# Optimization experiments

Hardware: AMD Instinct MI355X
Metric: run time of the kernel (lower is better)

Reference implementation:

```python
import jax, jax.numpy as jnp
import numpy as np

EPS = 1e-6
NUM_HEADS = 16

def _rmsnorm(h, w):
    hf = h.astype(jnp.float32)
    var = jnp.mean(hf * hf, axis=-1, keepdims=True)
    return (w * (hf * jax.lax.rsqrt(var + EPS))).astype(h.dtype)

def _rotary(t, cos, sin):
    # t: [B,N,H,hd]; cos/sin: [N, hd//2]
    tf = t.astype(jnp.float32)
    tr = tf[..., 0::2]
    ti = tf[..., 1::2]
    c = cos[None, :, None, :]
    s = sin[None, :, None, :]
    out_r = tr * c - ti * s
    out_i = tr * s + ti * c
    out = jnp.stack([out_r, out_i], axis=-1).reshape(t.shape)
    return out.astype(t.dtype)

def setup_inputs() -> dict:
    key = jax.random.key(0)
    ks = jax.random.split(key, 8)
    B, N, C = 2, 2048, 1024
    hd = C // NUM_HEADS
    x = jax.random.normal(ks[0], (B, N, C), jnp.float32)
    qkv_w = jax.random.normal(ks[1], (3 * C, C), jnp.float32) * (C ** -0.5)
    q_norm_w = jnp.ones((hd,), jnp.float32)
    k_norm_w = jnp.ones((hd,), jnp.float32)
    proj_w = jax.random.normal(ks[2], (C, C), jnp.float32) * (C ** -0.5)
    proj_b = jnp.zeros((C,), jnp.float32)
    # rotary freqs_cis = exp(i * theta): unit-magnitude cos/sin
    inv_freq = 1.0 / (10000.0 ** (jnp.arange(0, hd, 2, dtype=jnp.float32) / hd))
    ang = jnp.arange(N, dtype=jnp.float32)[:, None] * inv_freq[None, :]
    pos_cos = jnp.cos(ang)
    pos_sin = jnp.sin(ang)
    mask = jnp.tril(jnp.ones((N, N), dtype=bool))
    return {"x": x, "qkv_w": qkv_w, "q_norm_w": q_norm_w, "k_norm_w": k_norm_w,
            "proj_w": proj_w, "proj_b": proj_b, "pos_cos": pos_cos,
            "pos_sin": pos_sin, "mask": mask}

def reference(x, qkv_w, q_norm_w, k_norm_w, proj_w, proj_b, pos_cos, pos_sin, mask):
    B, N, C = x.shape
    H = NUM_HEADS
    hd = C // H
    qkv = (x @ qkv_w.T).reshape(B, N, 3, H, hd)
    q, k, v = qkv[:, :, 0], qkv[:, :, 1], qkv[:, :, 2]  # [B,N,H,hd]
    q = _rmsnorm(q, q_norm_w)
    k = _rmsnorm(k, k_norm_w)
    q = _rotary(q, pos_cos, pos_sin)
    k = _rotary(k, pos_cos, pos_sin)
    q = q.transpose(0, 2, 1, 3)  # [B,H,N,hd]
    k = k.transpose(0, 2, 1, 3)
    v = v.transpose(0, 2, 1, 3)
    scale = hd ** -0.5
    scores = jnp.einsum('bhqd,bhkd->bhqk', q, k) * scale
    scores = jnp.where(mask[None, None, :, :], scores, jnp.float32(-1e30))
    attn = jax.nn.softmax(scores, axis=-1)
    out = jnp.einsum('bhqk,bhkd->bhqd', attn, v)
    out = out.transpose(0, 2, 1, 3).reshape(B, N, C)
    return out @ proj_w.T + proj_b
```

## Files before the change

### kernel.cpp

```cpp
#include <hip/hip_runtime.h>

using u16 = unsigned short;
using short4v = __attribute__((ext_vector_type(4))) short;
using short8 = __attribute__((ext_vector_type(8))) short;
using floatx4 = __attribute__((ext_vector_type(4))) float;

__device__ __forceinline__ float bf2f(u16 h) {
  union { unsigned int u; float f; } v;
  v.u = ((unsigned int)h) << 16;
  return v.f;
}
__device__ __forceinline__ u16 f2bf(float f) {
  union { float f; unsigned int u; } v;
  v.f = f;
  unsigned int u = v.u;
  return (u16)((u + 0x7FFFu + ((u >> 16) & 1u)) >> 16);
}
__device__ __forceinline__ u16 f2bf_rtz(float f) {
  union { float f; unsigned int u; } v;
  v.f = f;
  return (u16)(v.u >> 16);
}

typedef const __attribute__((address_space(1))) unsigned int* gas_t;
typedef __attribute__((address_space(3))) unsigned int* las_t;
__device__ __forceinline__ void gl_lds16(const u16* g, u16* l) {
  __builtin_amdgcn_global_load_lds((gas_t)(const void*)g, (las_t)(void*)l, 16,
                                   0, 0);
}

#define QSCALE 0.180336880111f
#define EXPBIAS 23.0831206542f

__global__ __launch_bounds__(256) void cvt_all(
    const float* __restrict__ x, const float* __restrict__ wq,
    const float* __restrict__ wp, u16* __restrict__ xb, u16* __restrict__ wqb,
    u16* __restrict__ wpb) {
  int i = blockIdx.x * 256 + threadIdx.x;
  const float* src;
  u16* dst;
  int off;
  if (i < 1048576) {
    src = x; dst = xb; off = i;
  } else if (i < 1048576 + 786432) {
    src = wq; dst = wqb; off = i - 1048576;
  } else {
    src = wp; dst = wpb; off = i - 1835008;
  }
  float4 v = ((const float4*)src)[off];
  ushort4 o;
  o.x = f2bf(v.x);
  o.y = f2bf(v.y);
  o.z = f2bf(v.z);
  o.w = f2bf(v.w);
  ((ushort4*)dst)[off] = o;
}

template <int BIAS, int OUTBF16, int MT>
__global__ __launch_bounds__(256) void gemm_nt(
    const u16* __restrict__ A, const u16* __restrict__ B,
    const float* __restrict__ bias, void* __restrict__ Cout,
    int M, int N, int K) {
  constexpr int ROWS_A = MT * 32;
  __shared__ u16 As[ROWS_A * 32];
  __shared__ u16 Bs[128 * 32];
  const int tid = threadIdx.x;
  const int lane = tid & 63;
  const int wave = tid >> 6;
  const int col = lane & 15;
  const int quad = lane >> 4;
  const int bm = blockIdx.y * ROWS_A;
  const int bn = blockIdx.x * 128;
  const int wm = (wave >> 1) * (MT * 16);
  const int wn = (wave & 1) * 64;

  floatx4 acc[MT][4] = {};

  for (int kb = 0; kb < K; kb += 32) {
    __syncthreads();
#pragma unroll
    for (int c = tid; c < ROWS_A * 4; c += 256)
      gl_lds16(A + (size_t)(bm + (c >> 2)) * K + kb + (c & 3) * 8, As + c * 8);
#pragma unroll
    for (int c = tid; c < 512; c += 256)
      gl_lds16(B + (size_t)(bn + (c >> 2)) * K + kb + (c & 3) * 8, Bs + c * 8);
    __syncthreads();

    short8 af[MT], bfr[4];
#pragma unroll
    for (int i = 0; i < MT; i++)
      af[i] = *(const short8*)(As + (wm + i * 16 + col) * 32 + quad * 8);
#pragma unroll
    for (int i = 0; i < 4; i++)
      bfr[i] = *(const short8*)(Bs + (wn + i * 16 + col) * 32 + quad * 8);
#pragma unroll
    for (int mi = 0; mi < MT; mi++)
#pragma unroll
      for (int ni = 0; ni < 4; ni++)
        acc[mi][ni] = __builtin_amdgcn_mfma_f32_16x16x32_bf16(
            af[mi], bfr[ni], acc[mi][ni], 0, 0, 0);
  }

#pragma unroll
  for (int mi = 0; mi < MT; mi++) {
#pragma unroll
    for (int ni = 0; ni < 4; ni++) {
#pragma unroll
      for (int r = 0; r < 4; r++) {
        int row = bm + wm + mi * 16 + quad * 4 + r;
        int c = bn + wn + ni * 16 + col;
        float v = acc[mi][ni][r];
        if (BIAS) v += bias[c];
        if (OUTBF16)
          ((u16*)Cout)[(size_t)row * N + c] = f2bf(v);
        else
          ((float*)Cout)[(size_t)row * N + c] = v;
      }
    }
  }
}

__global__ __launch_bounds__(256) void rope_v(
    const u16* __restrict__ qkv, const float* __restrict__ qw,
    const float* __restrict__ kw, const float* __restrict__ pcos,
    const float* __restrict__ psin, u16* __restrict__ Qb,
    u16* __restrict__ Kb, u16* __restrict__ Vt) {
  __shared__ u16 T[64 * 68];
  const int bh = blockIdx.x;
  const int n0 = blockIdx.y * 64;
  const int b = bh >> 4, h = bh & 15;
  const int tid = threadIdx.x;
  const int lane = tid & 63;
  const int wave = tid >> 6;

  const float qwl = qw[lane];
  const float kwl = kw[lane];
  for (int tt = 0; tt < 16; tt++) {
    const int n = n0 + wave * 16 + tt;
    const int t = b * 2048 + n;
    const u16* base = qkv + (size_t)t * 3072 + h * 64 + lane;
    float qv = bf2f(base[0]);
    float kv = bf2f(base[1024]);

    float sq = qv * qv, sk = kv * kv;
#pragma unroll
    for (int off = 32; off; off >>= 1) {
      sq += __shfl_xor(sq, off);
      sk += __shfl_xor(sk, off);
    }
    float qn = qv * rsqrtf(sq * (1.0f / 64.0f) + 1e-6f) * qwl;
    float kn = kv * rsqrtf(sk * (1.0f / 64.0f) + 1e-6f) * kwl;

    const int i = lane >> 1;
    const float c = pcos[n * 32 + i];
    const float s = psin[n * 32 + i];
    float qp = __shfl_xor(qn, 1);
    float kp = __shfl_xor(kn, 1);
    float qr, kr;
    if (lane & 1) {
      qr = qp * s + qn * c;
      kr = kp * s + kn * c;
    } else {
      qr = qn * c - qp * s;
      kr = kn * c - kp * s;
    }
    qr *= QSCALE;

    const size_t o = ((size_t)bh * 2048 + n) * 64 + lane;
    Qb[o] = f2bf(qr);
    Kb[o] = f2bf(kr);
  }

  const int q = tid & 7;
  const int r = tid >> 3;
#pragma unroll
  for (int rr = r; rr < 64; rr += 32) {
    short8 v = *(const short8*)(qkv + (size_t)(b * 2048 + n0 + rr) * 3072 +
                                2048 + h * 64 + q * 8);
    *(short8*)&T[rr * 68 + q * 8] = v;
  }
  __syncthreads();
#pragma unroll
  for (int dd = r; dd < 64; dd += 32) {
    short8 o;
#pragma unroll
    for (int j = 0; j < 8; j++) o[j] = T[(q * 8 + j) * 68 + dd];
    *(short8*)(Vt + (size_t)(bh * 64 + dd) * 2048 + n0 + q * 8) = o;
  }
}

#define PSTR 68
__global__ __launch_bounds__(256) void attn_flash(
    const u16* __restrict__ Q, const u16* __restrict__ Kk,
    const u16* __restrict__ Vt, u16* __restrict__ O) {
  __shared__ u16 Ks[2][64 * 32];
  __shared__ u16 Vs[2][64 * 32];
  __shared__ u16 Pb[4][16 * PSTR];
  const int id = blockIdx.x;
  const int bh = id & 31;
  const int tile = 31 - (id >> 5);
  const int tid = threadIdx.x;
  const int lane = tid & 63;
  const int wave = tid >> 6;
  const int col = lane & 15;
  const int quad = lane >> 4;
  const int srow = tid >> 2;
  const int spc = (tid & 3) * 8;

  const u16* Qh = Q + (size_t)bh * 2048 * 64;
  const u16* Kh = Kk + (size_t)bh * 2048 * 64;
  const u16* Vh = Vt + (size_t)bh * 64 * 2048;
  const int b = bh >> 4, h = bh & 15;

  const int q0 = tile * 64 + wave * 16;

  short8 aq[2];
#pragma unroll
  for (int ks = 0; ks < 2; ks++)
    aq[ks] = *(const short8*)(Qh + (size_t)(q0 + col) * 64 + ks * 32 + quad * 8);

  floatx4 accO[4] = {};
  float ll = 0.0f;
  const int nsteps = tile + 1;

  for (int kt = 0; kt < nsteps; kt++) {
    const int j0 = kt * 64;
    __syncthreads();
#pragma unroll
    for (int half = 0; half < 2; half++) {
      gl_lds16(Kh + (size_t)(j0 + srow) * 64 + half * 32 + spc,
               &Ks[half][0] + tid * 8);
      gl_lds16(Vh + (size_t)srow * 2048 + j0 + half * 32 + spc,
               &Vs[half][0] + tid * 8);
    }
    __syncthreads();

    floatx4 s[4] = {};
#pragma unroll
    for (int nt = 0; nt < 4; nt++) {
#pragma unroll
      for (int ks = 0; ks < 2; ks++) {
        short8 bk = *(const short8*)&Ks[ks][(nt * 16 + col) * 32 + quad * 8];
        s[nt] =
            __builtin_amdgcn_mfma_f32_16x16x32_bf16(bk, aq[ks], s[nt], 0, 0, 0);
      }
    }

    if (j0 + 63 <= q0) {
#pragma unroll
      for (int nt = 0; nt < 4; nt++) {
        short4v pk;
#pragma unroll
        for (int r = 0; r < 4; r++) {
          float pv = exp2f(s[nt][r] - EXPBIAS);
          ll += pv;
          pk[r] = (short)f2bf_rtz(pv);
        }
        *(short4v*)&Pb[wave][col * PSTR + nt * 16 + quad * 4] = pk;
      }
    } else {
      const int qg = q0 + col;
#pragma unroll
      for (int nt = 0; nt < 4; nt++) {
        const int jgb = j0 + nt * 16 + quad * 4;
        short4v pk;
#pragma unroll
        for (int r = 0; r < 4; r++) {
          float pv = (jgb + r <= qg) ? exp2f(s[nt][r] - EXPBIAS) : 0.0f;
          ll += pv;
          pk[r] = (short)f2bf_rtz(pv);
        }
        *(short4v*)&Pb[wave][col * PSTR + nt * 16 + quad * 4] = pk;
      }
    }

    short8 ap[2];
#pragma unroll
    for (int kf = 0; kf < 2; kf++)
      ap[kf] = *(const short8*)&Pb[wave][col * PSTR + kf * 32 + quad * 8];
#pragma unroll
    for (int nt = 0; nt < 4; nt++) {
#pragma unroll
      for (int kf = 0; kf < 2; kf++) {
        short8 bv = *(const short8*)&Vs[kf][(nt * 16 + col) * 32 + quad * 8];
        accO[nt] =
            __builtin_amdgcn_mfma_f32_16x16x32_bf16(ap[kf], bv, accO[nt], 0, 0, 0);
      }
    }
  }

  ll += __shfl_xor(ll, 16);
  ll += __shfl_xor(ll, 32);
  float lrec[4];
#pragma unroll
  for (int r = 0; r < 4; r++) lrec[r] = 1.0f / __shfl(ll, quad * 4 + r);

#pragma unroll
  for (int nt = 0; nt < 4; nt++) {
#pragma unroll
    for (int r = 0; r < 4; r++) {
      int qg = q0 + quad * 4 + r;
      int d = nt * 16 + col;
      O[((size_t)(b * 2048 + qg) * 16 + h) * 64 + d] =
          f2bf(accO[nt][r] * lrec[r]);
    }
  }
}

extern "C" void kernel_launch(void* const* d_in, const int* in_sizes, int n_in,
                              void* d_out, int out_size, void* d_ws,
                              size_t ws_size, hipStream_t stream) {
  const float* x = (const float*)d_in[0];
  const float* qkv_w = (const float*)d_in[1];
  const float* q_norm_w = (const float*)d_in[2];
  const float* k_norm_w = (const float*)d_in[3];
  const float* proj_w = (const float*)d_in[4];
  const float* proj_b = (const float*)d_in[5];
  const float* pos_cos = (const float*)d_in[6];
  const float* pos_sin = (const float*)d_in[7];

  char* ws = (char*)d_ws;
  u16* xb = (u16*)ws;
  u16* wqkvb = (u16*)(ws + 8388608);
  u16* wprojb = (u16*)(ws + 14680064);
  u16* qkv = (u16*)(ws + 16777216);
  u16* Qb = (u16*)(ws + 41943040);
  u16* Kb = (u16*)(ws + 50331648);
  u16* Vt = (u16*)(ws + 58720256);
  u16* AO = (u16*)(ws + 67108864);

  cvt_all<<<8192, 256, 0, stream>>>(x, qkv_w, proj_w, xb, wqkvb, wprojb);

  gemm_nt<0, 1, 4><<<dim3(24, 32), 256, 0, stream>>>(xb, wqkvb, nullptr, qkv,
                                                     4096, 3072, 1024);

  rope_v<<<dim3(32, 32), 256, 0, stream>>>(qkv, q_norm_w, k_norm_w, pos_cos,
                                           pos_sin, Qb, Kb, Vt);

  attn_flash<<<dim3(1024), 256, 0, stream>>>(Qb, Kb, Vt, AO);

  gemm_nt<1, 0, 2><<<dim3(8, 64), 256, 0, stream>>>(AO, wprojb, proj_b,
                                                    (float*)d_out, 4096, 1024,
                                                    1024);
}
```

Before: 216.0 us.

## Fuse QK RMSNorm and rotary embedding into the QKV GEMM epilogue

Adds a dedicated QKV GEMM whose epilogue does per-head RMSNorm (shuffle reduction across the 16-lane column groups), applies rotary, and writes Q and K straight into head-major layout. Only V goes to a raw buffer, and a slimmed kernel transposes it. This removes the round trip of the full bf16 QKV tensor through global memory and one kernel's read pass. In exchange the epilogue is heavier, with scattered cos/sin loads and 2-byte stores, and the norm now runs on fp32 accumulators instead of bf16-rounded values.

```diff
diff --git a/kernel.cpp b/kernel.cpp
--- a/kernel.cpp
+++ b/kernel.cpp
@@ -54,6 +54,107 @@
   o.z = f2bf(v.z);
   o.w = f2bf(v.w);
   ((ushort4*)dst)[off] = o;
+}
+
+__global__ __launch_bounds__(256) void gemm_qkv(
+    const u16* __restrict__ A, const u16* __restrict__ B,
+    const float* __restrict__ qw, const float* __restrict__ kw,
+    const float* __restrict__ pcos, const float* __restrict__ psin,
+    u16* __restrict__ Qb, u16* __restrict__ Kb, u16* __restrict__ Vraw) {
+  __shared__ u16 As[128 * 32];
+  __shared__ u16 Bs[128 * 32];
+  const int tid = threadIdx.x;
+  const int lane = tid & 63;
+  const int wave = tid >> 6;
+  const int col = lane & 15;
+  const int quad = lane >> 4;
+  const int bm = blockIdx.y * 128;
+  const int bn = blockIdx.x * 128;
+  const int wm = (wave >> 1) * 64;
+  const int wn = (wave & 1) * 64;
+  const int K = 1024;
+
+  floatx4 acc[4][4] = {};
+
+  for (int kb = 0; kb < K; kb += 32) {
+    __syncthreads();
+#pragma unroll
+    for (int i = 0; i < 2; i++) {
+      const int c = i * 256 + tid;
+      const int row = c >> 2;
+      const int kc = (c & 3) * 8;
+      gl_lds16(A + (size_t)(bm + row) * K + kb + kc, As + c * 8);
+      gl_lds16(B + (size_t)(bn + row) * K + kb + kc, Bs + c * 8);
+    }
+    __syncthreads();
+
+    short8 af[4], bfr[4];
+#pragma unroll
+    for (int i = 0; i < 4; i++)
+      af[i] = *(const short8*)(As + (wm + i * 16 + col) * 32 + quad * 8);
+#pragma unroll
+    for (int i = 0; i < 4; i++)
+      bfr[i] = *(const short8*)(Bs + (wn + i * 16 + col) * 32 + quad * 8);
+#pragma unroll
+    for (int mi = 0; mi < 4; mi++)
+#pragma unroll
+      for (int ni = 0; ni < 4; ni++)
+        acc[mi][ni] = __builtin_amdgcn_mfma_f32_16x16x32_bf16(
+            af[mi], bfr[ni], acc[mi][ni], 0, 0, 0);
+  }
+
+  const int region = (int)blockIdx.x >> 3;
+
+  if (region == 2) {
+    const int c0 = ((int)blockIdx.x - 16) * 128 + wn;
+#pragma unroll
+    for (int mi = 0; mi < 4; mi++)
+#pragma unroll
+      for (int ni = 0; ni < 4; ni++)
+#pragma unroll
+        for (int r = 0; r < 4; r++) {
+          int row = bm + wm + mi * 16 + quad * 4 + r;
+          Vraw[(size_t)row * 1024 + c0 + ni * 16 + col] = f2bf(acc[mi][ni][r]);
+        }
+  } else {
+    const float* w = region ? kw : qw;
+    u16* Out = region ? Kb : Qb;
+    const int hh = (((int)blockIdx.x & 7) * 128 + wn) >> 6;
+    const int bb = bm >> 11;
+    const int bh = bb * 16 + hh;
+    const int nbase = (bm & 2047) + wm;
+    float wl[4];
+#pragma unroll
+    for (int ni = 0; ni < 4; ni++) wl[ni] = w[ni * 16 + col];
+
+#pragma unroll
+    for (int mi = 0; mi < 4; mi++) {
+#pragma unroll
+      for (int r = 0; r < 4; r++) {
+        float ssq = 0.0f;
+#pragma unroll
+        for (int ni = 0; ni < 4; ni++) ssq += acc[mi][ni][r] * acc[mi][ni][r];
+        ssq += __shfl_xor(ssq, 1);
+        ssq += __shfl_xor(ssq, 2);
+        ssq += __shfl_xor(ssq, 4);
+        ssq += __shfl_xor(ssq, 8);
+        const float rms = rsqrtf(ssq * (1.0f / 64.0f) + 1e-6f);
+        const int n = nbase + mi * 16 + quad * 4 + r;
+        u16* orow = Out + ((size_t)bh * 2048 + n) * 64;
+#pragma unroll
+        for (int ni = 0; ni < 4; ni++) {
+          const int d = ni * 16 + col;
+          float v = acc[mi][ni][r] * rms * wl[ni];
+          const float cc = pcos[n * 32 + (d >> 1)];
+          const float ss = psin[n * 32 + (d >> 1)];
+          const float vp = __shfl_xor(v, 1);
+          float o = (col & 1) ? (vp * ss + v * cc) : (v * cc - vp * ss);
+          if (region == 0) o *= QSCALE;
+          orow[d] = f2bf(o);
+        }
+      }
+    }
+  }
 }
 
 template <int BIAS, int OUTBF16, int MT>
@@ -120,63 +221,20 @@
   }
 }
 
-__global__ __launch_bounds__(256) void rope_v(
-    const u16* __restrict__ qkv, const float* __restrict__ qw,
-    const float* __restrict__ kw, const float* __restrict__ pcos,
-    const float* __restrict__ psin, u16* __restrict__ Qb,
-    u16* __restrict__ Kb, u16* __restrict__ Vt) {
+__global__ __launch_bounds__(256) void vtrans(const u16* __restrict__ Vraw,
+                                              u16* __restrict__ Vt) {
   __shared__ u16 T[64 * 68];
   const int bh = blockIdx.x;
   const int n0 = blockIdx.y * 64;
   const int b = bh >> 4, h = bh & 15;
   const int tid = threadIdx.x;
-  const int lane = tid & 63;
-  const int wave = tid >> 6;
-
-  const float qwl = qw[lane];
-  const float kwl = kw[lane];
-  for (int tt = 0; tt < 16; tt++) {
-    const int n = n0 + wave * 16 + tt;
-    const int t = b * 2048 + n;
-    const u16* base = qkv + (size_t)t * 3072 + h * 64 + lane;
-    float qv = bf2f(base[0]);
-    float kv = bf2f(base[1024]);
-
-    float sq = qv * qv, sk = kv * kv;
-#pragma unroll
-    for (int off = 32; off; off >>= 1) {
-      sq += __shfl_xor(sq, off);
-      sk += __shfl_xor(sk, off);
-    }
-    float qn = qv * rsqrtf(sq * (1.0f / 64.0f) + 1e-6f) * qwl;
-    float kn = kv * rsqrtf(sk * (1.0f / 64.0f) + 1e-6f) * kwl;
-
-    const int i = lane >> 1;
-    const float c = pcos[n * 32 + i];
-    const float s = psin[n * 32 + i];
-    float qp = __shfl_xor(qn, 1);
-    float kp = __shfl_xor(kn, 1);
-    float qr, kr;
-    if (lane & 1) {
-      qr = qp * s + qn * c;
-      kr = kp * s + kn * c;
-    } else {
-      qr = qn * c - qp * s;
-      kr = kn * c - kp * s;
-    }
-    qr *= QSCALE;
-
-    const size_t o = ((size_t)bh * 2048 + n) * 64 + lane;
-    Qb[o] = f2bf(qr);
-    Kb[o] = f2bf(kr);
-  }
-
   const int q = tid & 7;
   const int r = tid >> 3;
+
 #pragma unroll
   for (int rr = r; rr < 64; rr += 32) {
-    short8 v = *(const short8*)(qkv + (size_t)(b * 2048 + n0 + rr) * 3072 +
-                                2048 + h * 64 + q * 8);
+    short8 v = *(const short8*)(Vraw + (size_t)(b * 2048 + n0 + rr) * 1024 +
+                                h * 64 + q * 8);
     *(short8*)&T[rr * 68 + q * 8] = v;
   }
   __syncthreads();
@@ -323,19 +381,18 @@
   u16* xb = (u16*)ws;
   u16* wqkvb = (u16*)(ws + 8388608);
   u16* wprojb = (u16*)(ws + 14680064);
-  u16* qkv = (u16*)(ws + 16777216);
-  u16* Qb = (u16*)(ws + 41943040);
-  u16* Kb = (u16*)(ws + 50331648);
-  u16* Vt = (u16*)(ws + 58720256);
-  u16* AO = (u16*)(ws + 67108864);
+  u16* Vraw = (u16*)(ws + 16777216);
+  u16* Qb = (u16*)(ws + 25165824);
+  u16* Kb = (u16*)(ws + 33554432);
+  u16* Vt = (u16*)(ws + 41943040);
+  u16* AO = (u16*)(ws + 50331648);
 
   cvt_all<<<8192, 256, 0, stream>>>(x, qkv_w, proj_w, xb, wqkvb, wprojb);
 
-  gemm_nt<0, 1, 4><<<dim3(24, 32), 256, 0, stream>>>(xb, wqkvb, nullptr, qkv,
-                                                     4096, 3072, 1024);
-
-  rope_v<<<dim3(32, 32), 256, 0, stream>>>(qkv, q_norm_w, k_norm_w, pos_cos,
-                                           pos_sin, Qb, Kb, Vt);
+  gemm_qkv<<<dim3(24, 32), 256, 0, stream>>>(xb, wqkvb, q_norm_w, k_norm_w,
+                                             pos_cos, pos_sin, Qb, Kb, Vraw);
+
+  vtrans<<<dim3(32, 32), 256, 0, stream>>>(Vraw, Vt);
 
   attn_flash<<<dim3(1024), 256, 0, stream>>>(Qb, Kb, Vt, AO);
 
```

After: 220.6 us. 2.1% more time.
